# Optimization experiments

Hardware: AMD Instinct MI355X
Metric: run time of the kernel (lower is better)

The kernel has to match this reference:

```python
import jax, jax.numpy as jnp
import numpy as np
from jax import lax

B, T, DEPTH = 512, 32, 512
RNN, NCC = 512, 128
D_IN = DEPTH * (T * DEPTH // T // DEPTH) * 1 + NCC  # slice_len=1 -> 512 + 128 = 640


def setup_inputs() -> dict:
    key = jax.random.key(0)
    ks = jax.random.split(key, 7)
    s = 0.05  # tf.random_normal_initializer default stddev
    return {
        "f_pool": jax.random.normal(ks[0], (B, T, DEPTH), jnp.float32),
        "ground_truth": jax.random.normal(ks[1], (B, T, NCC), jnp.float32),
        "kernel": jax.random.normal(ks[2], (DEPTH + NCC, 4 * RNN), jnp.float32) * s,
        "rec_kernel": jax.random.normal(ks[3], (RNN, 4 * RNN), jnp.float32) * s,
        "bias": jax.random.normal(ks[4], (4 * RNN,), jnp.float32) * s,
        "softmax_w": jax.random.normal(ks[5], (RNN, NCC), jnp.float32) * s,
        "softmax_b": jax.random.normal(ks[6], (NCC,), jnp.float32) * s,
    }


def reference(f_pool, ground_truth, kernel, rec_kernel, bias, softmax_w, softmax_b):
    b, features_num, depth = f_pool.shape
    seq_length = ground_truth.shape[1]
    ncc = softmax_b.shape[0]
    rnn = rec_kernel.shape[0]
    slice_len = features_num // seq_length  # == 1 here
    gt_t = jnp.transpose(ground_truth, (1, 0, 2))  # [T, B, C] for scan

    def step(carry, inp):
        h, c, prev = carry
        t, gt_row = inp
        # image feature slice at char index t -> [B, slice_len*depth]
        feat = lax.dynamic_slice_in_dim(f_pool, t, slice_len, axis=1)
        feat = feat.reshape(b, slice_len * depth)
        x = jnp.concatenate([feat, prev], axis=1)
        z = x @ kernel + h @ rec_kernel + bias  # [B, 4*rnn]
        i, f, g, o = jnp.split(z, 4, axis=1)    # keras LSTMCell gate order
        c2 = jax.nn.sigmoid(f) * c + jax.nn.sigmoid(i) * jnp.tanh(g)
        h2 = jax.nn.sigmoid(o) * jnp.tanh(c2)
        logits = h2 @ softmax_w + softmax_b
        onehot = jax.nn.one_hot(jnp.argmax(logits, axis=1), ncc, dtype=f_pool.dtype)
        # teacher forcing: prev_output = ground_truth[:, t, :]
        return (h2, c2, gt_row), onehot

    h0 = jnp.zeros((b, rnn), f_pool.dtype)
    c0 = jnp.zeros((b, rnn), f_pool.dtype)
    prev0 = jnp.zeros((b, ncc), f_pool.dtype)
    (h, c, _), outs = lax.scan(step, (h0, c0, prev0), (jnp.arange(seq_length), gt_t))
    sequence_output = jnp.transpose(outs, (1, 0, 2))  # [B, T, C]
    return (sequence_output, h, c)
```

## Files before the change

kernel.cpp:

```cpp
#include <hip/hip_runtime.h>
#include <math.h>

typedef float  f32x4  __attribute__((ext_vector_type(4)));
typedef short  short8v __attribute__((ext_vector_type(8)));
typedef unsigned short ushort8v __attribute__((ext_vector_type(8)));
typedef unsigned short ushort2v __attribute__((ext_vector_type(2)));

#define KP_PRE 1920
#define KP_HS  1536

#define WAITV(N) asm volatile("s_waitcnt vmcnt(" #N ")" ::: "memory")
#define SBAR()   asm volatile("s_barrier" ::: "memory")

__device__ unsigned short g_Xb[16384][1920];
__device__ unsigned short g_Wb[2048][1920];
__device__ unsigned short g_Rb[2048][1536];
__device__ unsigned short g_hs[2][512][1536];
__device__ float g_pre[16384][2048];
__device__ float g_hf[2][512 * 512];
__device__ float g_swT[128][512];
__device__ float g_bperm[2048];
__device__ float g_plv[2][512 * 8];
__device__ int   g_pli[2][512 * 8];
__device__ unsigned g_xcnt[128];
__device__ unsigned g_xrel[128];

__global__ void init_counters()
{
    int t = threadIdx.x;
    if (t < 8) { g_xcnt[t * 16] = 0u; g_xrel[t * 16] = 0u; }
}

__device__ __forceinline__ unsigned short f2bf(float f) {
    unsigned u = __float_as_uint(f);
    return (unsigned short)((u + 0x7fffu + ((u >> 16) & 1u)) >> 16);
}
__device__ __forceinline__ float bf2f(unsigned short s) {
    return __uint_as_float(((unsigned)s) << 16);
}
__device__ __forceinline__ float sigf(float x) { return 1.f / (1.f + expf(-x)); }

__device__ __forceinline__ void split3(float v, unsigned short& s0,
                                       unsigned short& s1, unsigned short& s2) {
    s0 = f2bf(v); float f0 = bf2f(s0);
    s1 = f2bf(v - f0); float f1 = bf2f(s1);
    s2 = f2bf(v - f0 - f1);
}

__device__ __forceinline__ void gl16(const unsigned short* g, unsigned short* l) {
    __builtin_amdgcn_global_load_lds((const __attribute__((address_space(1))) void*)g,
                                     (__attribute__((address_space(3))) void*)l, 16, 0, 0);
}

__device__ __forceinline__ short8v fragld(const unsigned short* sh, int row, int uw) {
    return *(const short8v*)(sh + row * 64 + ((uw ^ (row & 7)) << 3));
}

__device__ __forceinline__ void stage_pre(const unsigned short* Ag,
                                          const unsigned short* Bg,
                                          int kr, unsigned short* slot, int tid)
{
#pragma unroll
    for (int s = 0; s < 3; ++s)
#pragma unroll
        for (int v = 0; v < 2; ++v) {
            int e = v * 512 + tid;
            gl16(Ag + (size_t)(e >> 3) * KP_PRE + s * 640 + kr * 64 + (e & 7) * 8,
                 slot + s * 8192 + e * 8);
        }
#pragma unroll
    for (int s = 0; s < 3; ++s) {
        int e = tid;
        gl16(Bg + (size_t)(e >> 3) * KP_PRE + s * 640 + kr * 64 + (e & 7) * 8,
             slot + 24576 + s * 4096 + e * 8);
    }
}

__device__ __forceinline__ void stageA3w(const unsigned short* Ag, int kr,
                                         unsigned short* buf, int tid)
{
#pragma unroll
    for (int s = 0; s < 3; ++s) {
        int e = tid;
        gl16(Ag + (size_t)(e >> 3) * KP_HS + (s * 8 + kr) * 64 + (e & 7) * 8,
             buf + s * 4096 + e * 8);
    }
}
__device__ __forceinline__ void stageB3w(const unsigned short* Bg, int kr,
                                         unsigned short* buf, int tid)
{
#pragma unroll
    for (int s = 0; s < 3; ++s) {
        int e = tid;
        gl16(Bg + (size_t)(e >> 3) * KP_HS + (s * 8 + kr) * 64 + (e & 7) * 8,
             buf + 12288 + s * 4096 + e * 8);
    }
}
__device__ __forceinline__ void stage6w(const unsigned short* Ag,
                                        const unsigned short* Bg,
                                        int kr, unsigned short* buf, int tid)
{
    stageA3w(Ag, kr, buf, tid);
    stageB3w(Bg, kr, buf, tid);
}

__global__ __launch_bounds__(256) void build_Xb(const float* __restrict__ fp,
                                                const float* __restrict__ gt)
{
    const int tid = threadIdx.x;
    const int m  = blockIdx.x * 16 + (tid >> 4);
    const int k8 = (blockIdx.y * 16 + (tid & 15)) * 8;
    const int t = m >> 9, b = m & 511;
    float x[8];
    if (k8 < 512) {
        float4 v0 = *(const float4*)(fp + ((size_t)(b * 32 + t)) * 512 + k8);
        float4 v1 = *(const float4*)(fp + ((size_t)(b * 32 + t)) * 512 + k8 + 4);
        x[0]=v0.x; x[1]=v0.y; x[2]=v0.z; x[3]=v0.w;
        x[4]=v1.x; x[5]=v1.y; x[6]=v1.z; x[7]=v1.w;
    } else if (t > 0) {
        float4 v0 = *(const float4*)(gt + ((size_t)(b * 32 + t - 1)) * 128 + (k8 - 512));
        float4 v1 = *(const float4*)(gt + ((size_t)(b * 32 + t - 1)) * 128 + (k8 - 512) + 4);
        x[0]=v0.x; x[1]=v0.y; x[2]=v0.z; x[3]=v0.w;
        x[4]=v1.x; x[5]=v1.y; x[6]=v1.z; x[7]=v1.w;
    } else {
#pragma unroll
        for (int j = 0; j < 8; ++j) x[j] = 0.f;
    }
    unsigned short s0[8], s1[8], s2[8];
#pragma unroll
    for (int j = 0; j < 8; ++j) split3(x[j], s0[j], s1[j], s2[j]);
    const int u = (k8 >> 3) & 7;
    const int base = (k8 & ~63) + (((u ^ (m & 7))) << 3);
    ushort8v v0, v1, v2;
#pragma unroll
    for (int j = 0; j < 8; ++j) { v0[j] = s0[j]; v1[j] = s1[j]; v2[j] = s2[j]; }
    *(ushort8v*)&g_Xb[m][0 * 640 + base] = v0;
    *(ushort8v*)&g_Xb[m][1 * 640 + base] = v1;
    *(ushort8v*)&g_Xb[m][2 * 640 + base] = v2;
}

__global__ __launch_bounds__(256) void build_Wb(const float* __restrict__ Wk)
{
    const int tid = threadIdx.x;
    const int np = blockIdx.x * 16 + (tid >> 4);
    const int k8 = (blockIdx.y * 16 + (tid & 15)) * 8;
    const int n = (np & 3) * 512 + (np >> 2);
    float x[8];
#pragma unroll
    for (int j = 0; j < 8; ++j) x[j] = Wk[(size_t)(k8 + j) * 2048 + n];
    unsigned short s0[8], s1[8], s2[8];
#pragma unroll
    for (int j = 0; j < 8; ++j) split3(x[j], s0[j], s1[j], s2[j]);
    const int u = (k8 >> 3) & 7;
    const int base = (k8 & ~63) + (((u ^ (np & 7))) << 3);
    ushort8v v0, v1, v2;
#pragma unroll
    for (int j = 0; j < 8; ++j) { v0[j] = s0[j]; v1[j] = s1[j]; v2[j] = s2[j]; }
    *(ushort8v*)&g_Wb[np][0 * 640 + base] = v0;
    *(ushort8v*)&g_Wb[np][1 * 640 + base] = v1;
    *(ushort8v*)&g_Wb[np][2 * 640 + base] = v2;
}

__global__ __launch_bounds__(256) void build_Rb(const float* __restrict__ Rk)
{
    const int tid = threadIdx.x;
    const int np = blockIdx.x * 16 + (tid >> 4);
    const int k8 = (blockIdx.y * 16 + (tid & 15)) * 8;
    const int n = (np & 3) * 512 + (np >> 2);
    float x[8];
#pragma unroll
    for (int j = 0; j < 8; ++j) x[j] = Rk[(size_t)(k8 + j) * 2048 + n];
    unsigned short s0[8], s1[8], s2[8];
#pragma unroll
    for (int j = 0; j < 8; ++j) split3(x[j], s0[j], s1[j], s2[j]);
    const int u = (k8 >> 3) & 7;
    const int base = (k8 & ~63) + (((u ^ (np & 7))) << 3);
    ushort8v v0, v1, v2;
#pragma unroll
    for (int j = 0; j < 8; ++j) { v0[j] = s0[j]; v1[j] = s1[j]; v2[j] = s2[j]; }
    *(ushort8v*)&g_Rb[np][0 * 512 + base] = v0;
    *(ushort8v*)&g_Rb[np][1 * 512 + base] = v1;
    *(ushort8v*)&g_Rb[np][2 * 512 + base] = v2;
}

__global__ __launch_bounds__(256) void build_misc(const float* __restrict__ sw,
                                                  const float* __restrict__ bias)
{
    int id = blockIdx.x * 256 + threadIdx.x;
    if (id < 128 * 512) {
        int c = id >> 9, r = id & 511;
        g_swT[c][r] = sw[(size_t)r * 128 + c];
    } else if (id < 128 * 512 + 2048) {
        int np = id - 128 * 512;
        g_bperm[np] = bias[(np & 3) * 512 + (np >> 2)];
    }
}

__global__ __launch_bounds__(512, 1) void pre_mfma()
{
    __shared__ __align__(16) char smem[147456];
    const int tid = threadIdx.x, lane = tid & 63, wave = tid >> 6;
    const int vid = blockIdx.y * 32 + blockIdx.x;
    const int x8 = vid & 7, k = vid >> 3;
    const int m0 = (x8 + 8 * (k >> 5)) * 128;
    const int n0 = (k & 31) * 64;
    const int wr = wave >> 2, wc = wave & 3, l15 = lane & 15, ql = lane >> 4;
    unsigned short* ring = (unsigned short*)smem;
    const unsigned short* Ag = &g_Xb[m0][0];
    const unsigned short* Bg = &g_Wb[n0][0];

    constexpr int ipt[6] = {0, 0, 1, 0, 1, 2};
    constexpr int jpt[6] = {0, 1, 0, 2, 1, 0};

    f32x4 acc[4];
#pragma unroll
    for (int a = 0; a < 4; ++a) acc[a] = (f32x4){0.f, 0.f, 0.f, 0.f};

    stage_pre(Ag, Bg, 0, ring, tid);
    stage_pre(Ag, Bg, 1, ring + 36864, tid);
    for (int kr = 0; kr < 10; ++kr) {
        if (kr <= 8) WAITV(9);
        else         WAITV(0);
        SBAR();
        const unsigned short* Ab = ring + (kr & 1) * 36864;
        const unsigned short* Bb = Ab + 24576;
#pragma unroll
        for (int sub = 0; sub < 2; ++sub) {
            const int uw = sub * 4 + ql;
            short8v a0[4], a1[4], a2[4], b0, b1, b2;
#pragma unroll
            for (int fa = 0; fa < 4; ++fa) {
                a0[fa] = fragld(Ab + 0 * 8192, wr * 64 + fa * 16 + l15, uw);
                a1[fa] = fragld(Ab + 1 * 8192, wr * 64 + fa * 16 + l15, uw);
                a2[fa] = fragld(Ab + 2 * 8192, wr * 64 + fa * 16 + l15, uw);
            }
            b0 = fragld(Bb + 0 * 4096, wc * 16 + l15, uw);
            b1 = fragld(Bb + 1 * 4096, wc * 16 + l15, uw);
            b2 = fragld(Bb + 2 * 4096, wc * 16 + l15, uw);
#pragma unroll
            for (int p = 0; p < 6; ++p) {
                const short8v* A2 = (ipt[p] == 0) ? a0 : ((ipt[p] == 1) ? a1 : a2);
                const short8v  B2 = (jpt[p] == 0) ? b0 : ((jpt[p] == 1) ? b1 : b2);
#pragma unroll
                for (int fa = 0; fa < 4; ++fa)
                    acc[fa] = __builtin_amdgcn_mfma_f32_16x16x32_bf16(
                        A2[fa], B2, acc[fa], 0, 0, 0);
            }
        }
        SBAR();
        if (kr + 2 < 10)
            stage_pre(Ag, Bg, kr + 2, ring + (kr & 1) * 36864, tid);
    }
#pragma unroll
    for (int fa = 0; fa < 4; ++fa) {
        const int np = n0 + wc * 16 + l15;
        const float bv = g_bperm[np];
#pragma unroll
        for (int q = 0; q < 4; ++q) {
            const int m = m0 + wr * 64 + fa * 16 + ql * 4 + q;
            g_pre[m][np] = acc[fa][q] + bv;
        }
    }
}

__global__ __launch_bounds__(512, 1) void charnn_rec(
    const float* __restrict__ sb,
    float* __restrict__ seq, float* __restrict__ out_h, float* __restrict__ out_c)
{
    __shared__ __align__(16) char smem[147456];
    float (*zbuf)[68] = (float (*)[68])smem;
    unsigned short* ring = (unsigned short*)smem;

    const int bi = blockIdx.x, tid = threadIdx.x;
    const int lane = tid & 63, wave = tid >> 6;
    const int x  = bi & 7, jj = bi >> 3;
    const int Mg = x;
    const int Ng = jj;
    const int m0 = Mg * 64, n0 = Ng * 64;
    const int wr = wave >> 2, wc = wave & 3, l15 = lane & 15, ql = lane >> 4;

    const int m_e = tid >> 3;
    const int rb2 = (tid & 7) * 2;
    const int mg = m0 + m_e;
    float cst[2] = {0.f, 0.f};

    const int rgrp = Mg * 4 + (jj & 3);
    const int cg   = jj >> 2;
    const int arow = Mg * 64 + jj * 2;
    const bool xleader = (jj == 0);

    constexpr int ipt[6] = {0, 0, 1, 0, 1, 2};
    constexpr int jpt[6] = {0, 1, 0, 2, 1, 0};

    const unsigned short* Bg = &g_Rb[n0][0];

    f32x4 pqa, pqb;
    {
        const float* prow = &g_pre[0 * 512 + mg][n0];
        pqa = *(const f32x4*)(prow + rb2 * 4);
        pqb = *(const f32x4*)(prow + rb2 * 4 + 4);
    }

    for (int ph = 0; ph < 34; ++ph) {
        const int t = ph;
        const bool do_z = (ph >= 1 && ph <= 31);

        const unsigned short* Ag = nullptr;
        if (do_z) {
            Ag = &g_hs[(t + 1) & 1][m0][0];
            stageA3w(Ag, 0, ring + 0 * 24576, tid);
            stageA3w(Ag, 1, ring + 1 * 24576, tid);
            stageA3w(Ag, 2, ring + 2 * 24576, tid);
        }

        if (ph >= 1 && ph <= 32 && tid < 256) {
            const int tl = ph - 1;
            const int row = rgrp * 16 + (tid >> 4);
            const int col = cg * 16 + (tid & 15);
            const float* hrow = &g_hf[tl & 1][(size_t)row * 512];
            const float* wcol = &g_swT[col][0];
            float s0 = sb[col], s1 = 0.f, s2 = 0.f, s3 = 0.f;
#pragma unroll 8
            for (int k = 0; k < 512; k += 4) {
                float4 hv = *(const float4*)(hrow + k);
                float4 wv = *(const float4*)(wcol + k);
                s0 = fmaf(hv.x, wv.x, s0); s1 = fmaf(hv.y, wv.y, s1);
                s2 = fmaf(hv.z, wv.z, s2); s3 = fmaf(hv.w, wv.w, s3);
            }
            float bv = (s0 + s1) + (s2 + s3); int bidx = col;
#pragma unroll
            for (int m = 1; m < 16; m <<= 1) {
                float ov = __shfl_xor(bv, m, 64);
                int   oi = __shfl_xor(bidx, m, 64);
                if (ov > bv || (ov == bv && oi < bidx)) { bv = ov; bidx = oi; }
            }
            if ((tid & 15) == 0) {
                g_plv[tl & 1][row * 8 + cg] = bv;
                g_pli[tl & 1][row * 8 + cg] = bidx;
            }
        }

        if (ph >= 2 && wave < 2) {
            const int t2 = ph - 2;
            const int row = arow + wave;
            float v; int idx;
            if (lane < 8) {
                v   = g_plv[t2 & 1][row * 8 + lane];
                idx = g_pli[t2 & 1][row * 8 + lane];
            } else { v = -INFINITY; idx = 0x7fffffff; }
#pragma unroll
            for (int m = 1; m < 8; m <<= 1) {
                float ov = __shfl_xor(v, m, 64);
                int   oi = __shfl_xor(idx, m, 64);
                if (ov > v || (ov == v && oi < idx)) { v = ov; idx = oi; }
            }
            int win = __shfl(idx, 0, 64);
            if (lane < 32) {
                int c4 = lane * 4;
                float4 o;
                o.x = (c4 + 0 == win) ? 1.f : 0.f;
                o.y = (c4 + 1 == win) ? 1.f : 0.f;
                o.z = (c4 + 2 == win) ? 1.f : 0.f;
                o.w = (c4 + 3 == win) ? 1.f : 0.f;
                *(float4*)(seq + ((size_t)row * 32 + t2) * 128 + c4) = o;
            }
        }

        if (ph <= 31) {
            if (do_z) {
                f32x4 acc[2];
                acc[0] = (f32x4){0.f, 0.f, 0.f, 0.f};
                acc[1] = (f32x4){0.f, 0.f, 0.f, 0.f};
#pragma unroll
                for (int kr = 0; kr < 8; ++kr) {
                    if (kr >= 1 && kr <= 5)
                        stage6w(Ag, Bg, kr + 2, ring + ((kr + 2) % 3) * 24576, tid);
                    if      (kr == 0) WAITV(6);
                    else if (kr == 1) WAITV(9);
                    else if (kr == 6) WAITV(6);
                    else if (kr == 7) WAITV(0);
                    else              WAITV(12);
                    SBAR();
                    const unsigned short* Ab = ring + (kr % 3) * 24576;
                    const unsigned short* Bb = Ab + 12288;
#pragma unroll
                    for (int sub = 0; sub < 2; ++sub) {
                        const int uw = sub * 4 + ql;
                        short8v a0[2], a1[2], a2[2], b0, b1, b2;
                        a0[0] = fragld(Ab + 0 * 4096, wr * 32 + l15, uw);
                        a0[1] = fragld(Ab + 0 * 4096, wr * 32 + 16 + l15, uw);
                        a1[0] = fragld(Ab + 1 * 4096, wr * 32 + l15, uw);
                        a1[1] = fragld(Ab + 1 * 4096, wr * 32 + 16 + l15, uw);
                        a2[0] = fragld(Ab + 2 * 4096, wr * 32 + l15, uw);
                        a2[1] = fragld(Ab + 2 * 4096, wr * 32 + 16 + l15, uw);
                        b0 = fragld(Bb + 0 * 4096, wc * 16 + l15, uw);
                        b1 = fragld(Bb + 1 * 4096, wc * 16 + l15, uw);
                        b2 = fragld(Bb + 2 * 4096, wc * 16 + l15, uw);
#pragma unroll
                        for (int p = 0; p < 6; ++p) {
                            const short8v* A2 = (ipt[p] == 0) ? a0 :
                                                ((ipt[p] == 1) ? a1 : a2);
                            const short8v  B2 = (jpt[p] == 0) ? b0 :
                                                ((jpt[p] == 1) ? b1 : b2);
                            acc[0] = __builtin_amdgcn_mfma_f32_16x16x32_bf16(
                                A2[0], B2, acc[0], 0, 0, 0);
                            acc[1] = __builtin_amdgcn_mfma_f32_16x16x32_bf16(
                                A2[1], B2, acc[1], 0, 0, 0);
                        }
                    }
                }
                __syncthreads();
#pragma unroll
                for (int fa = 0; fa < 2; ++fa)
#pragma unroll
                    for (int q2 = 0; q2 < 4; ++q2)
                        zbuf[wr * 32 + fa * 16 + ql * 4 + q2]
                            [wc * 16 + l15] = acc[fa][q2];
            }
            __syncthreads();

            unsigned short hs0[2], hs1[2], hs2[2];
            float hv2[2];
#pragma unroll
            for (int i = 0; i < 2; ++i) {
                const int rl = rb2 + i;
                float zi, zf, zg, zo;
                if (t > 0) {
                    float4 zq = *(const float4*)&zbuf[m_e][rl * 4];
                    zi = zq.x; zf = zq.y; zg = zq.z; zo = zq.w;
                } else { zi = zf = zg = zo = 0.f; }
                f32x4 pq = (i == 0) ? pqa : pqb;
                zi += pq[0]; zf += pq[1]; zg += pq[2]; zo += pq[3];
                float c2 = sigf(zf) * cst[i] + sigf(zi) * tanhf(zg);
                float h2 = sigf(zo) * tanhf(c2);
                cst[i] = c2;
                hv2[i] = h2;
                split3(h2, hs0[i], hs1[i], hs2[i]);
            }
            const int r0g = Ng * 16 + rb2;
            *(float2*)&g_hf[t & 1][(size_t)mg * 512 + r0g] =
                make_float2(hv2[0], hv2[1]);
            if (t == 31) {
                *(float2*)&out_h[(size_t)mg * 512 + r0g] =
                    make_float2(hv2[0], hv2[1]);
                *(float2*)&out_c[(size_t)mg * 512 + r0g] =
                    make_float2(cst[0], cst[1]);
            }
            const int su = ((r0g >> 3) & 7) ^ (mg & 7);
            const int abase = (r0g & ~63) + (su << 3) + (r0g & 7);
#pragma unroll
            for (int i = 0; i < 3; ++i) {
                ushort2v v;
#pragma unroll
                for (int j = 0; j < 2; ++j)
                    v[j] = (i == 0) ? hs0[j] : ((i == 1) ? hs1[j] : hs2[j]);
                *(ushort2v*)&g_hs[t & 1][mg][i * 512 + abase] = v;
            }
        }

        if (ph < 33) {
            __syncthreads();

            if (ph <= 30) {
                stageB3w(Bg, 0, ring + 0 * 24576, tid);
                stageB3w(Bg, 1, ring + 1 * 24576, tid);
                stageB3w(Bg, 2, ring + 2 * 24576, tid);
                const float* prow = &g_pre[(ph + 1) * 512 + mg][n0];
                pqa = *(const f32x4*)(prow + rb2 * 4);
                pqb = *(const f32x4*)(prow + rb2 * 4 + 4);
            }

            if (tid == 0) {
                __hip_atomic_fetch_add(&g_xcnt[x * 16], 1u,
                                       __ATOMIC_RELAXED, __HIP_MEMORY_SCOPE_AGENT);
                if (xleader) {
                    const unsigned xt = 32u * (unsigned)(ph + 1);
                    while (__hip_atomic_load(&g_xcnt[x * 16], __ATOMIC_RELAXED,
                                             __HIP_MEMORY_SCOPE_AGENT) < xt)
                        __builtin_amdgcn_s_sleep(2);
                    __hip_atomic_store(&g_xrel[x * 16], (unsigned)(ph + 1),
                                       __ATOMIC_RELAXED, __HIP_MEMORY_SCOPE_AGENT);
                }
                while (__hip_atomic_load(&g_xrel[x * 16], __ATOMIC_RELAXED,
                                         __HIP_MEMORY_SCOPE_AGENT) < (unsigned)(ph + 1))
                    __builtin_amdgcn_s_sleep(2);
                __builtin_amdgcn_fence(__ATOMIC_ACQUIRE, "agent");
            }
            __syncthreads();
        }
    }
}

extern "C" void kernel_launch(void* const* d_in, const int* in_sizes, int n_in,
                              void* d_out, int out_size, void* d_ws, size_t ws_size,
                              hipStream_t stream)
{
    const float* fp   = (const float*)d_in[0];
    const float* gt   = (const float*)d_in[1];
    const float* Wk   = (const float*)d_in[2];
    const float* Rk   = (const float*)d_in[3];
    const float* bias = (const float*)d_in[4];
    const float* sw   = (const float*)d_in[5];
    const float* sb   = (const float*)d_in[6];
    float* seq   = (float*)d_out;
    float* out_h = seq + (size_t)512 * 32 * 128;
    float* out_c = out_h + (size_t)512 * 512;

    hipLaunchKernelGGL(init_counters, dim3(1), dim3(64), 0, stream);
    hipLaunchKernelGGL(build_Xb, dim3(1024, 5), dim3(256), 0, stream, fp, gt);
    hipLaunchKernelGGL(build_Wb, dim3(128, 5), dim3(256), 0, stream, Wk);
    hipLaunchKernelGGL(build_Rb, dim3(128, 4), dim3(256), 0, stream, Rk);
    hipLaunchKernelGGL(build_misc, dim3(264), dim3(256), 0, stream, sw, bias);
    hipLaunchKernelGGL(pre_mfma, dim3(32, 128), dim3(512), 0, stream);
    hipLaunchKernelGGL(charnn_rec, dim3(256), dim3(512), 0, stream,
                       sb, seq, out_h, out_c);
}
```

Before: 1.425 ms.

## Merge setup kernels into one launch and make pre-GEMM persistent over N tiles

The five preparation kernels (counter init, X/W/R bf16 split, softmax transpose and bias permute) are merged into a single launch that dispatches work by block index range. The input-projection GEMM changes from 4096 one-tile blocks to 256 persistent blocks, each sweeping 16 N tiles for a fixed M tile with a continuous double-buffered pipeline across tile boundaries. This removes launch overhead and per-tile pipeline prologue and epilogue costs. In exchange, far fewer blocks may underuse the GPU's compute units, and the A tile is still reloaded for every N tile, so nothing is reused across tiles. Unused constant tables are also added.

```diff
diff --git a/kernel.cpp b/kernel.cpp
--- a/kernel.cpp
+++ b/kernel.cpp
@@ -25,12 +25,6 @@
 __device__ unsigned g_xcnt[128];
 __device__ unsigned g_xrel[128];
 
-__global__ void init_counters()
-{
-    int t = threadIdx.x;
-    if (t < 8) { g_xcnt[t * 16] = 0u; g_xrel[t * 16] = 0u; }
-}
-
 __device__ __forceinline__ unsigned short f2bf(float f) {
     unsigned u = __float_as_uint(f);
     return (unsigned short)((u + 0x7fffu + ((u >> 16) & 1u)) >> 16);
@@ -47,6 +41,9 @@
     s2 = f2bf(v - f0 - f1);
 }
 
+__device__ __constant__ int c_ipt[6] = {0, 0, 1, 0, 1, 2};
+__device__ __constant__ int c_jpt[6] = {0, 1, 0, 2, 1, 0};
+
 __device__ __forceinline__ void gl16(const unsigned short* g, unsigned short* l) {
     __builtin_amdgcn_global_load_lds((const __attribute__((address_space(1))) void*)g,
                                      (__attribute__((address_space(3))) void*)l, 16, 0, 0);
@@ -104,95 +101,96 @@
     stageB3w(Bg, kr, buf, tid);
 }
 
-__global__ __launch_bounds__(256) void build_Xb(const float* __restrict__ fp,
-                                                const float* __restrict__ gt)
-{
-    const int tid = threadIdx.x;
-    const int m  = blockIdx.x * 16 + (tid >> 4);
-    const int k8 = (blockIdx.y * 16 + (tid & 15)) * 8;
-    const int t = m >> 9, b = m & 511;
-    float x[8];
-    if (k8 < 512) {
-        float4 v0 = *(const float4*)(fp + ((size_t)(b * 32 + t)) * 512 + k8);
-        float4 v1 = *(const float4*)(fp + ((size_t)(b * 32 + t)) * 512 + k8 + 4);
-        x[0]=v0.x; x[1]=v0.y; x[2]=v0.z; x[3]=v0.w;
-        x[4]=v1.x; x[5]=v1.y; x[6]=v1.z; x[7]=v1.w;
-    } else if (t > 0) {
-        float4 v0 = *(const float4*)(gt + ((size_t)(b * 32 + t - 1)) * 128 + (k8 - 512));
-        float4 v1 = *(const float4*)(gt + ((size_t)(b * 32 + t - 1)) * 128 + (k8 - 512) + 4);
-        x[0]=v0.x; x[1]=v0.y; x[2]=v0.z; x[3]=v0.w;
-        x[4]=v1.x; x[5]=v1.y; x[6]=v1.z; x[7]=v1.w;
+__global__ __launch_bounds__(256) void build_all(const float* __restrict__ fp,
+                                                 const float* __restrict__ gt,
+                                                 const float* __restrict__ Wk,
+                                                 const float* __restrict__ Rk,
+                                                 const float* __restrict__ sw,
+                                                 const float* __restrict__ bias)
+{
+    const int b = blockIdx.x, tid = threadIdx.x;
+    if (b < 5120) {
+        const int bx = b & 1023, by = b >> 10;
+        const int m  = bx * 16 + (tid >> 4);
+        const int k8 = (by * 16 + (tid & 15)) * 8;
+        const int t = m >> 9, bb = m & 511;
+        float x[8];
+        if (k8 < 512) {
+            float4 v0 = *(const float4*)(fp + ((size_t)(bb * 32 + t)) * 512 + k8);
+            float4 v1 = *(const float4*)(fp + ((size_t)(bb * 32 + t)) * 512 + k8 + 4);
+            x[0]=v0.x; x[1]=v0.y; x[2]=v0.z; x[3]=v0.w;
+            x[4]=v1.x; x[5]=v1.y; x[6]=v1.z; x[7]=v1.w;
+        } else if (t > 0) {
+            float4 v0 = *(const float4*)(gt + ((size_t)(bb * 32 + t - 1)) * 128 + (k8 - 512));
+            float4 v1 = *(const float4*)(gt + ((size_t)(bb * 32 + t - 1)) * 128 + (k8 - 512) + 4);
+            x[0]=v0.x; x[1]=v0.y; x[2]=v0.z; x[3]=v0.w;
+            x[4]=v1.x; x[5]=v1.y; x[6]=v1.z; x[7]=v1.w;
+        } else {
+#pragma unroll
+            for (int j = 0; j < 8; ++j) x[j] = 0.f;
+        }
+        unsigned short s0[8], s1[8], s2[8];
+#pragma unroll
+        for (int j = 0; j < 8; ++j) split3(x[j], s0[j], s1[j], s2[j]);
+        const int u = (k8 >> 3) & 7;
+        const int base = (k8 & ~63) + (((u ^ (m & 7))) << 3);
+        ushort8v v0, v1, v2;
+#pragma unroll
+        for (int j = 0; j < 8; ++j) { v0[j] = s0[j]; v1[j] = s1[j]; v2[j] = s2[j]; }
+        *(ushort8v*)&g_Xb[m][0 * 640 + base] = v0;
+        *(ushort8v*)&g_Xb[m][1 * 640 + base] = v1;
+        *(ushort8v*)&g_Xb[m][2 * 640 + base] = v2;
+    } else if (b < 5760) {
+        const int ib = b - 5120;
+        const int bx = ib & 127, by = ib >> 7;
+        const int np = bx * 16 + (tid >> 4);
+        const int k8 = (by * 16 + (tid & 15)) * 8;
+        const int n = (np & 3) * 512 + (np >> 2);
+        float x[8];
+#pragma unroll
+        for (int j = 0; j < 8; ++j) x[j] = Wk[(size_t)(k8 + j) * 2048 + n];
+        unsigned short s0[8], s1[8], s2[8];
+#pragma unroll
+        for (int j = 0; j < 8; ++j) split3(x[j], s0[j], s1[j], s2[j]);
+        const int u = (k8 >> 3) & 7;
+        const int base = (k8 & ~63) + (((u ^ (np & 7))) << 3);
+        ushort8v v0, v1, v2;
+#pragma unroll
+        for (int j = 0; j < 8; ++j) { v0[j] = s0[j]; v1[j] = s1[j]; v2[j] = s2[j]; }
+        *(ushort8v*)&g_Wb[np][0 * 640 + base] = v0;
+        *(ushort8v*)&g_Wb[np][1 * 640 + base] = v1;
+        *(ushort8v*)&g_Wb[np][2 * 640 + base] = v2;
+    } else if (b < 6272) {
+        const int ib = b - 5760;
+        const int bx = ib & 127, by = ib >> 7;
+        const int np = bx * 16 + (tid >> 4);
+        const int k8 = (by * 16 + (tid & 15)) * 8;
+        const int n = (np & 3) * 512 + (np >> 2);
+        float x[8];
+#pragma unroll
+        for (int j = 0; j < 8; ++j) x[j] = Rk[(size_t)(k8 + j) * 2048 + n];
+        unsigned short s0[8], s1[8], s2[8];
+#pragma unroll
+        for (int j = 0; j < 8; ++j) split3(x[j], s0[j], s1[j], s2[j]);
+        const int u = (k8 >> 3) & 7;
+        const int base = (k8 & ~63) + (((u ^ (np & 7))) << 3);
+        ushort8v v0, v1, v2;
+#pragma unroll
+        for (int j = 0; j < 8; ++j) { v0[j] = s0[j]; v1[j] = s1[j]; v2[j] = s2[j]; }
+        *(ushort8v*)&g_Rb[np][0 * 512 + base] = v0;
+        *(ushort8v*)&g_Rb[np][1 * 512 + base] = v1;
+        *(ushort8v*)&g_Rb[np][2 * 512 + base] = v2;
+    } else if (b < 6536) {
+        int id = (b - 6272) * 256 + tid;
+        if (id < 128 * 512) {
+            int c = id >> 9, r = id & 511;
+            g_swT[c][r] = sw[(size_t)r * 128 + c];
+        } else if (id < 128 * 512 + 2048) {
+            int np = id - 128 * 512;
+            g_bperm[np] = bias[(np & 3) * 512 + (np >> 2)];
+        }
     } else {
-#pragma unroll
-        for (int j = 0; j < 8; ++j) x[j] = 0.f;
-    }
-    unsigned short s0[8], s1[8], s2[8];
-#pragma unroll
-    for (int j = 0; j < 8; ++j) split3(x[j], s0[j], s1[j], s2[j]);
-    const int u = (k8 >> 3) & 7;
-    const int base = (k8 & ~63) + (((u ^ (m & 7))) << 3);
-    ushort8v v0, v1, v2;
-#pragma unroll
-    for (int j = 0; j < 8; ++j) { v0[j] = s0[j]; v1[j] = s1[j]; v2[j] = s2[j]; }
-    *(ushort8v*)&g_Xb[m][0 * 640 + base] = v0;
-    *(ushort8v*)&g_Xb[m][1 * 640 + base] = v1;
-    *(ushort8v*)&g_Xb[m][2 * 640 + base] = v2;
-}
-
-__global__ __launch_bounds__(256) void build_Wb(const float* __restrict__ Wk)
-{
-    const int tid = threadIdx.x;
-    const int np = blockIdx.x * 16 + (tid >> 4);
-    const int k8 = (blockIdx.y * 16 + (tid & 15)) * 8;
-    const int n = (np & 3) * 512 + (np >> 2);
-    float x[8];
-#pragma unroll
-    for (int j = 0; j < 8; ++j) x[j] = Wk[(size_t)(k8 + j) * 2048 + n];
-    unsigned short s0[8], s1[8], s2[8];
-#pragma unroll
-    for (int j = 0; j < 8; ++j) split3(x[j], s0[j], s1[j], s2[j]);
-    const int u = (k8 >> 3) & 7;
-    const int base = (k8 & ~63) + (((u ^ (np & 7))) << 3);
-    ushort8v v0, v1, v2;
-#pragma unroll
-    for (int j = 0; j < 8; ++j) { v0[j] = s0[j]; v1[j] = s1[j]; v2[j] = s2[j]; }
-    *(ushort8v*)&g_Wb[np][0 * 640 + base] = v0;
-    *(ushort8v*)&g_Wb[np][1 * 640 + base] = v1;
-    *(ushort8v*)&g_Wb[np][2 * 640 + base] = v2;
-}
-
-__global__ __launch_bounds__(256) void build_Rb(const float* __restrict__ Rk)
-{
-    const int tid = threadIdx.x;
-    const int np = blockIdx.x * 16 + (tid >> 4);
-    const int k8 = (blockIdx.y * 16 + (tid & 15)) * 8;
-    const int n = (np & 3) * 512 + (np >> 2);
-    float x[8];
-#pragma unroll
-    for (int j = 0; j < 8; ++j) x[j] = Rk[(size_t)(k8 + j) * 2048 + n];
-    unsigned short s0[8], s1[8], s2[8];
-#pragma unroll
-    for (int j = 0; j < 8; ++j) split3(x[j], s0[j], s1[j], s2[j]);
-    const int u = (k8 >> 3) & 7;
-    const int base = (k8 & ~63) + (((u ^ (np & 7))) << 3);
-    ushort8v v0, v1, v2;
-#pragma unroll
-    for (int j = 0; j < 8; ++j) { v0[j] = s0[j]; v1[j] = s1[j]; v2[j] = s2[j]; }
-    *(ushort8v*)&g_Rb[np][0 * 512 + base] = v0;
-    *(ushort8v*)&g_Rb[np][1 * 512 + base] = v1;
-    *(ushort8v*)&g_Rb[np][2 * 512 + base] = v2;
-}
-
-__global__ __launch_bounds__(256) void build_misc(const float* __restrict__ sw,
-                                                  const float* __restrict__ bias)
-{
-    int id = blockIdx.x * 256 + threadIdx.x;
-    if (id < 128 * 512) {
-        int c = id >> 9, r = id & 511;
-        g_swT[c][r] = sw[(size_t)r * 128 + c];
-    } else if (id < 128 * 512 + 2048) {
-        int np = id - 128 * 512;
-        g_bperm[np] = bias[(np & 3) * 512 + (np >> 2)];
+        if (tid < 8) { g_xcnt[tid * 16] = 0u; g_xrel[tid * 16] = 0u; }
     }
 }
 
@@ -200,29 +198,34 @@
 {
     __shared__ __align__(16) char smem[147456];
     const int tid = threadIdx.x, lane = tid & 63, wave = tid >> 6;
-    const int vid = blockIdx.y * 32 + blockIdx.x;
-    const int x8 = vid & 7, k = vid >> 3;
-    const int m0 = (x8 + 8 * (k >> 5)) * 128;
-    const int n0 = (k & 31) * 64;
+    const int bi = blockIdx.x;
+    const int x8 = bi & 7, r = bi >> 3;
+    const int M  = x8 + 8 * (r >> 1);
+    const int half = r & 1;
+    const int m0 = M * 128;
     const int wr = wave >> 2, wc = wave & 3, l15 = lane & 15, ql = lane >> 4;
     unsigned short* ring = (unsigned short*)smem;
     const unsigned short* Ag = &g_Xb[m0][0];
-    const unsigned short* Bg = &g_Wb[n0][0];
 
     constexpr int ipt[6] = {0, 0, 1, 0, 1, 2};
     constexpr int jpt[6] = {0, 1, 0, 2, 1, 0};
 
     f32x4 acc[4];
-#pragma unroll
-    for (int a = 0; a < 4; ++a) acc[a] = (f32x4){0.f, 0.f, 0.f, 0.f};
-
-    stage_pre(Ag, Bg, 0, ring, tid);
-    stage_pre(Ag, Bg, 1, ring + 36864, tid);
-    for (int kr = 0; kr < 10; ++kr) {
-        if (kr <= 8) WAITV(9);
+
+    stage_pre(Ag, &g_Wb[(half * 16 + 0) * 64][0], 0, ring + 0 * 36864, tid);
+    stage_pre(Ag, &g_Wb[(half * 16 + 0) * 64][0], 1, ring + 1 * 36864, tid);
+    for (int c = 0; c < 160; ++c) {
+        const int kr = c - (c / 10) * 10;
+        const int tile = c / 10;
+        const int n0 = (half * 16 + tile) * 64;
+        if (kr == 0) {
+#pragma unroll
+            for (int a = 0; a < 4; ++a) acc[a] = (f32x4){0.f, 0.f, 0.f, 0.f};
+        }
+        if (c < 159) WAITV(9);
         else         WAITV(0);
         SBAR();
-        const unsigned short* Ab = ring + (kr & 1) * 36864;
+        const unsigned short* Ab = ring + (c & 1) * 36864;
         const unsigned short* Bb = Ab + 24576;
 #pragma unroll
         for (int sub = 0; sub < 2; ++sub) {
@@ -248,17 +251,23 @@
             }
         }
         SBAR();
-        if (kr + 2 < 10)
-            stage_pre(Ag, Bg, kr + 2, ring + (kr & 1) * 36864, tid);
-    }
-#pragma unroll
-    for (int fa = 0; fa < 4; ++fa) {
-        const int np = n0 + wc * 16 + l15;
-        const float bv = g_bperm[np];
-#pragma unroll
-        for (int q = 0; q < 4; ++q) {
-            const int m = m0 + wr * 64 + fa * 16 + ql * 4 + q;
-            g_pre[m][np] = acc[fa][q] + bv;
+        if (c + 2 < 160) {
+            const int c2 = c + 2;
+            const int t2 = c2 / 10;
+            stage_pre(Ag, &g_Wb[(half * 16 + t2) * 64][0], c2 - t2 * 10,
+                      ring + (c2 & 1) * 36864, tid);
+        }
+        if (kr == 9) {
+#pragma unroll
+            for (int fa = 0; fa < 4; ++fa) {
+                const int np = n0 + wc * 16 + l15;
+                const float bv = g_bperm[np];
+#pragma unroll
+                for (int q = 0; q < 4; ++q) {
+                    const int m = m0 + wr * 64 + fa * 16 + ql * 4 + q;
+                    g_pre[m][np] = acc[fa][q] + bv;
+                }
+            }
         }
     }
 }
@@ -506,12 +515,9 @@
     float* out_h = seq + (size_t)512 * 32 * 128;
     float* out_c = out_h + (size_t)512 * 512;
 
-    hipLaunchKernelGGL(init_counters, dim3(1), dim3(64), 0, stream);
-    hipLaunchKernelGGL(build_Xb, dim3(1024, 5), dim3(256), 0, stream, fp, gt);
-    hipLaunchKernelGGL(build_Wb, dim3(128, 5), dim3(256), 0, stream, Wk);
-    hipLaunchKernelGGL(build_Rb, dim3(128, 4), dim3(256), 0, stream, Rk);
-    hipLaunchKernelGGL(build_misc, dim3(264), dim3(256), 0, stream, sw, bias);
-    hipLaunchKernelGGL(pre_mfma, dim3(32, 128), dim3(512), 0, stream);
+    hipLaunchKernelGGL(build_all, dim3(6537), dim3(256), 0, stream,
+                       fp, gt, Wk, Rk, sw, bias);
+    hipLaunchKernelGGL(pre_mfma, dim3(256), dim3(512), 0, stream);
     hipLaunchKernelGGL(charnn_rec, dim3(256), dim3(512), 0, stream,
                        sb, seq, out_h, out_c);
 }
```

Result: faster. 1.382 ms (-3.0%).
